# Kernel tuning notes

Hardware: AMD Instinct MI355X
Metric: run time of the kernel (lower is better)

The kernel has to match this reference:

```python
import jax, jax.numpy as jnp
import numpy as np

B, H, S, DH = 2, 16, 2048, 64

def setup_inputs() -> dict:
    key = jax.random.key(0)
    k1, k2, k3 = jax.random.split(key, 3)
    return {
        "query": jax.random.normal(k1, (B, H, S, DH), dtype=jnp.float32),
        "key": jax.random.normal(k2, (B, H, S, DH), dtype=jnp.float32),
        "value": jax.random.normal(k3, (B, H, S, DH), dtype=jnp.float32),
        "key_padding_mask": jnp.zeros((B, S), dtype=bool),
    }

def reference(query, key, value, key_padding_mask):
    # scores: [B, H, Sq, Sk]
    scale = 1.0 / jnp.sqrt(jnp.asarray(query.shape[-1], query.dtype))
    scores = jnp.einsum("bhqd,bhkd->bhqk", query, key) * scale
    # key padding mask broadcasts over heads and query positions
    scores = jnp.where(key_padding_mask[:, None, None, :], -jnp.inf, scores)
    attn = jax.nn.softmax(scores, axis=-1)
    # dropout is identity in eval mode (deterministic reference)
    out = jnp.einsum("bhqk,bhkd->bhqd", attn, value)
    # [B, H, S, Dh] -> [B, S, H*Dh]
    b, h, s, dh = out.shape
    return out.transpose(0, 2, 1, 3).reshape(b, s, h * dh)
```

## Files before the change

### kernel.cpp

```cpp
#include <hip/hip_runtime.h>

typedef __attribute__((ext_vector_type(4))) float f32x4;
typedef __attribute__((ext_vector_type(4))) short s16x4;
typedef __attribute__((ext_vector_type(8))) short s16x8;

constexpr int Bn = 2, Hn = 16, Sn = 2048, DHn = 64;
constexpr int TQ = 64;
constexpr int TK = 64;
constexpr int NT = Sn / TK;
constexpr int TILE_SH = TK * DHn;
constexpr float SHIFT = 16.0f;

__device__ __forceinline__ unsigned pk2(float a, float b) {
  unsigned ua = __builtin_bit_cast(unsigned, a);
  unsigned ub = __builtin_bit_cast(unsigned, b);
  ua += 0x7fffu + ((ua >> 16) & 1u);
  ub += 0x7fffu + ((ub >> 16) & 1u);
  return (ua >> 16) | (ub & 0xffff0000u);
}

__device__ __forceinline__ unsigned cvtpk(float a, float b) {
  unsigned r;
  asm("v_cvt_pk_bf16_f32 %0, %1, %2" : "=v"(r) : "v"(a), "v"(b));
  return r;
}

__device__ __forceinline__ float fexp2(float x) {
#if __has_builtin(__builtin_amdgcn_exp2f)
  return __builtin_amdgcn_exp2f(x);
#else
  return exp2f(x);
#endif
}

__device__ __forceinline__ f32x4 mfma16(s16x4 a, s16x4 b, f32x4 c) {
#if __has_builtin(__builtin_amdgcn_mfma_f32_16x16x16bf16_1k)
  return __builtin_amdgcn_mfma_f32_16x16x16bf16_1k(a, b, c, 0, 0, 0);
#else
  asm("v_mfma_f32_16x16x16_bf16 %0, %1, %2, %0" : "+v"(c) : "v"(a), "v"(b));
  return c;
#endif
}

__global__ __launch_bounds__(256)
void prepack_kernel(const float* __restrict__ Kg, const float* __restrict__ Vg,
                    short* __restrict__ Kp, short* __restrict__ Vp) {
  const int blk = blockIdx.x;
  const int tid = threadIdx.x;
  const float* Kt = Kg + (size_t)blk * TILE_SH;
  const float* Vt = Vg + (size_t)blk * TILE_SH;
  short* Kd = Kp + (size_t)blk * TILE_SH;
  short* Vd = Vp + (size_t)blk * TILE_SH;

  {
    const int r = tid >> 2;
    const int cb = (tid & 3) * 2;
#pragma unroll
    for (int cc = 0; cc < 2; ++cc) {
      int c = cb + cc;
      const float4* p = (const float4*)(Kt + (size_t)r * DHn + c * 8);
      float4 x = p[0], y = p[1];
      union { unsigned u[4]; s16x8 v; } tmp;
      tmp.u[0] = pk2(x.x, x.y); tmp.u[1] = pk2(x.z, x.w);
      tmp.u[2] = pk2(y.x, y.y); tmp.u[3] = pk2(y.z, y.w);
      *(s16x8*)&Kd[r * 64 + (c ^ (r & 7)) * 8] = tmp.v;
    }
  }
  {
    const int d = tid & 63;
    const int kb = (tid >> 6) * 16;
#pragma unroll
    for (int cc = 0; cc < 2; ++cc) {
      int k0 = kb + cc * 8;
      float v0[8];
#pragma unroll
      for (int j = 0; j < 8; ++j) v0[j] = Vt[(size_t)(k0 + j) * DHn + d];
      union { unsigned u[4]; s16x8 v; } tmp;
      tmp.u[0] = pk2(v0[0], v0[1]); tmp.u[1] = pk2(v0[2], v0[3]);
      tmp.u[2] = pk2(v0[4], v0[5]); tmp.u[3] = pk2(v0[6], v0[7]);
      int c = k0 >> 3;
      *(s16x8*)&Vd[d * 64 + (c ^ (d & 7)) * 8] = tmp.v;
    }
  }
}

__global__ __launch_bounds__(256, 4)
void fattn_kernel(const float* __restrict__ Qg, const short* __restrict__ Kp,
                  const short* __restrict__ Vp, const unsigned char* __restrict__ maskg,
                  float* __restrict__ Og) {
  __shared__ __align__(16) float Obuf[TQ * DHn];
  __shared__ float Lb[2][TQ];

  const int tid  = threadIdx.x;
  const int w    = tid >> 6;
  const int lane = tid & 63;
  const int n    = lane & 15;
  const int q4   = lane >> 4;
  const int swz  = n & 7;
  const int wk   = w & 1;
  const int wq   = w >> 1;

  const int blk = blockIdx.x;
  const int bh  = blk & 31;
  const int qt  = blk >> 5;
  const int b   = bh >> 4;
  const int h   = bh & 15;

  const float* Qb = Qg + (size_t)bh * Sn * DHn;
  const short* Kt = Kp + (size_t)bh * NT * TILE_SH;
  const short* Vt = Vp + (size_t)bh * NT * TILE_SH;
  const unsigned char* mq = maskg + (size_t)b * Sn;

  const int q0w = qt * TQ + wq * 32;
  const int t0  = qt & (NT - 1);

  const float c1 = 0.125f * 1.4426950408889634f;
  s16x8 qf[2][2];
#pragma unroll
  for (int qg = 0; qg < 2; ++qg) {
    const float* qrow = Qb + (size_t)(q0w + qg * 16 + n) * DHn;
#pragma unroll
    for (int kc = 0; kc < 2; ++kc) {
      const float4* p = (const float4*)(qrow + kc * 32 + q4 * 8);
      float4 x = p[0], y = p[1];
      union { unsigned u[4]; s16x8 v; } tmp;
      tmp.u[0] = pk2(x.x * c1, x.y * c1);
      tmp.u[1] = pk2(x.z * c1, x.w * c1);
      tmp.u[2] = pk2(y.x * c1, y.y * c1);
      tmp.u[3] = pk2(y.z * c1, y.w * c1);
      qf[qg][kc] = tmp.v;
    }
  }

  const int c0    = q4 ^ swz;
  const int offA  = n * 64 + c0 * 8;
  const int offB  = n * 64 + (c0 ^ 4) * 8;
  const int kbase = wk * 2048;
  const int vsub = (q4 & 1) * 4;
  const int vch0 = (((wk * 4) + (q4 >> 1)) ^ swz) * 8;
  const int vch1 = (((wk * 4) + 2 + (q4 >> 1)) ^ swz) * 8;
  const int mb0  = wk * 32 + q4 * 4;

  f32x4 Oa[2][4];
#pragma unroll
  for (int qg = 0; qg < 2; ++qg)
#pragma unroll
    for (int na = 0; na < 4; ++na) Oa[qg][na] = (f32x4){0.f, 0.f, 0.f, 0.f};
  float lsum[2] = {0.f, 0.f};

  unsigned m0 = *(const unsigned*)&mq[t0 * 64 + mb0];
  unsigned m1 = *(const unsigned*)&mq[t0 * 64 + mb0 + 16];

  for (int i = 0; i < NT; ++i) {
    const int t = (t0 + i) & (NT - 1);
    const short* Ktile = Kt + (size_t)t * TILE_SH;
    const short* Vtile = Vt + (size_t)t * TILE_SH;

    s16x8 kf[2][2];
#pragma unroll
    for (int mc = 0; mc < 2; ++mc) {
      kf[mc][0] = *(const s16x8*)&Ktile[kbase + mc * 1024 + offA];
      kf[mc][1] = *(const s16x8*)&Ktile[kbase + mc * 1024 + offB];
    }
    s16x4 vf[4][2];
#pragma unroll
    for (int na = 0; na < 4; ++na) {
      vf[na][0] = *(const s16x4*)&Vtile[na * 1024 + n * 64 + vch0 + vsub];
      vf[na][1] = *(const s16x4*)&Vtile[na * 1024 + n * 64 + vch1 + vsub];
    }

    const int tn = (t0 + i + 1) & (NT - 1);
    const unsigned mn0 = *(const unsigned*)&mq[tn * 64 + mb0];
    const unsigned mn1 = *(const unsigned*)&mq[tn * 64 + mb0 + 16];

    f32x4 sa[2][2];
#pragma unroll
    for (int r = 0; r < 4; ++r) {
      float b0 = ((m0 >> (8 * r)) & 0xffu) ? -1e30f : -SHIFT;
      float b1 = ((m1 >> (8 * r)) & 0xffu) ? -1e30f : -SHIFT;
      sa[0][0][r] = b0; sa[0][1][r] = b1;
      sa[1][0][r] = b0; sa[1][1][r] = b1;
    }

    __builtin_amdgcn_s_setprio(1);
#pragma unroll
    for (int qg = 0; qg < 2; ++qg)
#pragma unroll
      for (int mc = 0; mc < 2; ++mc)
#pragma unroll
        for (int kc = 0; kc < 2; ++kc)
          sa[qg][mc] = __builtin_amdgcn_mfma_f32_16x16x32_bf16(kf[mc][kc], qf[qg][kc], sa[qg][mc], 0, 0, 0);
    __builtin_amdgcn_s_setprio(0);

    s16x4 pa[2][2];
#pragma unroll
    for (int qg = 0; qg < 2; ++qg) {
#pragma unroll
      for (int mc = 0; mc < 2; ++mc) {
        float p0 = fexp2(sa[qg][mc][0]);
        float p1 = fexp2(sa[qg][mc][1]);
        float p2 = fexp2(sa[qg][mc][2]);
        float p3 = fexp2(sa[qg][mc][3]);
        lsum[qg] += (p0 + p1) + (p2 + p3);
        union { unsigned u[2]; s16x4 v4; } pw;
        pw.u[0] = cvtpk(p0, p1);
        pw.u[1] = cvtpk(p2, p3);
        pa[qg][mc] = pw.v4;
      }
    }

    __builtin_amdgcn_s_setprio(1);
#pragma unroll
    for (int qg = 0; qg < 2; ++qg)
#pragma unroll
      for (int na = 0; na < 4; ++na)
#pragma unroll
        for (int mc = 0; mc < 2; ++mc)
          Oa[qg][na] = mfma16(pa[qg][mc], vf[na][mc], Oa[qg][na]);
    __builtin_amdgcn_s_setprio(0);

    m0 = mn0;
    m1 = mn1;
  }

  lsum[0] += __shfl_xor(lsum[0], 16); lsum[0] += __shfl_xor(lsum[0], 32);
  lsum[1] += __shfl_xor(lsum[1], 16); lsum[1] += __shfl_xor(lsum[1], 32);
  if (lane < 16) {
    Lb[wk][wq * 32 + lane]      = lsum[0];
    Lb[wk][wq * 32 + 16 + lane] = lsum[1];
  }
  if (wk == 1) {
#pragma unroll
    for (int qg = 0; qg < 2; ++qg)
#pragma unroll
      for (int r = 0; r < 4; ++r) {
        const int ql = wq * 32 + qg * 16 + q4 * 4 + r;
#pragma unroll
        for (int na = 0; na < 4; ++na)
          Obuf[ql * 64 + na * 16 + n] = Oa[qg][na][r];
      }
  }
  __syncthreads();
  if (wk == 0) {
#pragma unroll
    for (int qg = 0; qg < 2; ++qg) {
#pragma unroll
      for (int r = 0; r < 4; ++r) {
        const int ql = wq * 32 + qg * 16 + q4 * 4 + r;
        const float inv = 1.0f / (Lb[0][ql] + Lb[1][ql]);
        const int q = qt * TQ + ql;
        float* orow = Og + (size_t)(b * Sn + q) * (Hn * DHn) + h * DHn;
#pragma unroll
        for (int na = 0; na < 4; ++na)
          orow[na * 16 + n] = (Oa[qg][na][r] + Obuf[ql * 64 + na * 16 + n]) * inv;
      }
    }
  }
}

extern "C" void kernel_launch(void* const* d_in, const int* in_sizes, int n_in,
                              void* d_out, int out_size, void* d_ws, size_t ws_size,
                              hipStream_t stream) {
  (void)in_sizes; (void)n_in; (void)ws_size; (void)out_size;
  const float* Q = (const float*)d_in[0];
  const float* K = (const float*)d_in[1];
  const float* V = (const float*)d_in[2];
  const unsigned char* mask = (const unsigned char*)d_in[3];
  float* out = (float*)d_out;

  short* Kp = (short*)d_ws;
  short* Vp = Kp + (size_t)Bn * Hn * Sn * DHn;

  hipLaunchKernelGGL(prepack_kernel, dim3(Bn * Hn * NT), dim3(256), 0, stream, K, V, Kp, Vp);
  hipLaunchKernelGGL(fattn_kernel, dim3(Bn * Hn * (Sn / TQ)), dim3(256), 0, stream,
                     Q, Kp, Vp, mask, out);
}
```

Baseline: 169.6 us.

## Stage K/V tiles through LDS with double-buffered async global-to-LDS loads

Instead of each wave reading packed K/V fragments straight from global memory every iteration, each wave now streams its half of the next-but-one K/V tile into a private LDS double buffer using global_load_lds. Explicit waitcnt fences and sched barriers overlap those loads with the MFMA work. The mask row is also staged in LDS, and V is prepacked in a new 32-wide swizzled layout to match. This aims to hide global load latency, but it adds a lot of LDS (four ~18KB regions) and drops launch bounds occupancy from 4 to 2. The per-wave buffers mean each wave fetches its own copy, and the manual vmcnt accounting is fragile.

```diff
diff --git a/kernel.cpp b/kernel.cpp
--- a/kernel.cpp
+++ b/kernel.cpp
@@ -9,6 +9,7 @@
 constexpr int TK = 64;
 constexpr int NT = Sn / TK;
 constexpr int TILE_SH = TK * DHn;
+constexpr int WREG = 9216;
 constexpr float SHIFT = 16.0f;
 
 __device__ __forceinline__ unsigned pk2(float a, float b) {
@@ -31,6 +32,12 @@
 #else
   return exp2f(x);
 #endif
+}
+
+__device__ __forceinline__ void gl2lds16(const short* g, short* l) {
+  __builtin_amdgcn_global_load_lds(
+      (const __attribute__((address_space(1))) void*)g,
+      (__attribute__((address_space(3))) void*)l, 16, 0, 0);
 }
 
 __device__ __forceinline__ f32x4 mfma16(s16x4 a, s16x4 b, f32x4 c) {
@@ -78,25 +85,24 @@
       union { unsigned u[4]; s16x8 v; } tmp;
       tmp.u[0] = pk2(v0[0], v0[1]); tmp.u[1] = pk2(v0[2], v0[3]);
       tmp.u[2] = pk2(v0[4], v0[5]); tmp.u[3] = pk2(v0[6], v0[7]);
-      int c = k0 >> 3;
-      *(s16x8*)&Vd[d * 64 + (c ^ (d & 7)) * 8] = tmp.v;
-    }
-  }
-}
-
-__global__ __launch_bounds__(256, 4)
+      const int h  = k0 >> 5;
+      const int c2 = (k0 >> 3) & 3;
+      *(s16x8*)&Vd[h * 2048 + d * 32 + ((c2 ^ (d & 3)) * 8)] = tmp.v;
+    }
+  }
+}
+
+__global__ __launch_bounds__(256, 2)
 void fattn_kernel(const float* __restrict__ Qg, const short* __restrict__ Kp,
                   const short* __restrict__ Vp, const unsigned char* __restrict__ maskg,
                   float* __restrict__ Og) {
-  __shared__ __align__(16) float Obuf[TQ * DHn];
-  __shared__ float Lb[2][TQ];
+  __shared__ __align__(16) short Sall[4 * WREG];
 
   const int tid  = threadIdx.x;
   const int w    = tid >> 6;
   const int lane = tid & 63;
   const int n    = lane & 15;
   const int q4   = lane >> 4;
-  const int swz  = n & 7;
   const int wk   = w & 1;
   const int wq   = w >> 1;
 
@@ -113,6 +119,9 @@
 
   const int q0w = qt * TQ + wq * 32;
   const int t0  = qt & (NT - 1);
+
+  short* Wb = &Sall[w * WREG];
+  const unsigned char* Mw = (const unsigned char*)(Wb + 8192);
 
   const float c1 = 0.125f * 1.4426950408889634f;
   s16x8 qf[2][2];
@@ -132,13 +141,15 @@
     }
   }
 
-  const int c0    = q4 ^ swz;
-  const int offA  = n * 64 + c0 * 8;
-  const int offB  = n * 64 + (c0 ^ 4) * 8;
-  const int kbase = wk * 2048;
+  const int swz  = n & 7;
+  const int c0   = q4 ^ swz;
+  const int offA = n * 64 + c0 * 8;
+  const int offB = n * 64 + (c0 ^ 4) * 8;
+  const int vrow = n * 32;
+  const int vq   = q4 >> 1;
   const int vsub = (q4 & 1) * 4;
-  const int vch0 = (((wk * 4) + (q4 >> 1)) ^ swz) * 8;
-  const int vch1 = (((wk * 4) + 2 + (q4 >> 1)) ^ swz) * 8;
+  const int vch0 = ((vq ^ (n & 3)) * 8) + vsub;
+  const int vch1 = (((2 + vq) ^ (n & 3)) * 8) + vsub;
   const int mb0  = wk * 32 + q4 * 4;
 
   f32x4 Oa[2][4];
@@ -148,30 +159,72 @@
     for (int na = 0; na < 4; ++na) Oa[qg][na] = (f32x4){0.f, 0.f, 0.f, 0.f};
   float lsum[2] = {0.f, 0.f};
 
-  unsigned m0 = *(const unsigned*)&mq[t0 * 64 + mb0];
-  unsigned m1 = *(const unsigned*)&mq[t0 * 64 + mb0 + 16];
+  asm volatile("s_waitcnt vmcnt(0)" ::: "memory");
+#pragma unroll
+  for (int k = 0; k < 2; ++k)
+    gl2lds16((const short*)mq + k * 512 + lane * 8, Wb + 8192 + k * 512);
+  {
+    const short* Ktile = Kt + (size_t)t0 * TILE_SH;
+    const short* Vtile = Vt + (size_t)t0 * TILE_SH;
+#pragma unroll
+    for (int k = 0; k < 4; ++k)
+      gl2lds16(Ktile + wk * 2048 + k * 512 + lane * 8, Wb + k * 512);
+#pragma unroll
+    for (int k = 0; k < 4; ++k)
+      gl2lds16(Vtile + wk * 2048 + k * 512 + lane * 8, Wb + 2048 + k * 512);
+  }
+  {
+    const int t1 = (t0 + 1) & (NT - 1);
+    const short* Ktile = Kt + (size_t)t1 * TILE_SH;
+    const short* Vtile = Vt + (size_t)t1 * TILE_SH;
+#pragma unroll
+    for (int k = 0; k < 4; ++k)
+      gl2lds16(Ktile + wk * 2048 + k * 512 + lane * 8, Wb + 4096 + k * 512);
+#pragma unroll
+    for (int k = 0; k < 4; ++k)
+      gl2lds16(Vtile + wk * 2048 + k * 512 + lane * 8, Wb + 4096 + 2048 + k * 512);
+  }
+  asm volatile("s_waitcnt vmcnt(8)" ::: "memory");
+  __builtin_amdgcn_sched_barrier(0);
+
+  unsigned m0 = *(const unsigned*)&Mw[t0 * 64 + mb0];
+  unsigned m1 = *(const unsigned*)&Mw[t0 * 64 + mb0 + 16];
 
   for (int i = 0; i < NT; ++i) {
-    const int t = (t0 + i) & (NT - 1);
-    const short* Ktile = Kt + (size_t)t * TILE_SH;
-    const short* Vtile = Vt + (size_t)t * TILE_SH;
+    const int cur = i & 1;
+    const short* Ks = Wb + cur * 4096;
+    const short* Vs = Ks + 2048;
 
     s16x8 kf[2][2];
 #pragma unroll
     for (int mc = 0; mc < 2; ++mc) {
-      kf[mc][0] = *(const s16x8*)&Ktile[kbase + mc * 1024 + offA];
-      kf[mc][1] = *(const s16x8*)&Ktile[kbase + mc * 1024 + offB];
+      kf[mc][0] = *(const s16x8*)&Ks[mc * 1024 + offA];
+      kf[mc][1] = *(const s16x8*)&Ks[mc * 1024 + offB];
     }
     s16x4 vf[4][2];
 #pragma unroll
     for (int na = 0; na < 4; ++na) {
-      vf[na][0] = *(const s16x4*)&Vtile[na * 1024 + n * 64 + vch0 + vsub];
-      vf[na][1] = *(const s16x4*)&Vtile[na * 1024 + n * 64 + vch1 + vsub];
-    }
-
+      vf[na][0] = *(const s16x4*)&Vs[na * 512 + vrow + vch0];
+      vf[na][1] = *(const s16x4*)&Vs[na * 512 + vrow + vch1];
+    }
     const int tn = (t0 + i + 1) & (NT - 1);
-    const unsigned mn0 = *(const unsigned*)&mq[tn * 64 + mb0];
-    const unsigned mn1 = *(const unsigned*)&mq[tn * 64 + mb0 + 16];
+    const unsigned mn0 = *(const unsigned*)&Mw[tn * 64 + mb0];
+    const unsigned mn1 = *(const unsigned*)&Mw[tn * 64 + mb0 + 16];
+
+    asm volatile("s_waitcnt lgkmcnt(0)" ::: "memory");
+    __builtin_amdgcn_sched_barrier(0);
+
+    {
+      const int ts = (t0 + i + 2) & (NT - 1);
+      const short* Ktile = Kt + (size_t)ts * TILE_SH;
+      const short* Vtile = Vt + (size_t)ts * TILE_SH;
+#pragma unroll
+      for (int k = 0; k < 4; ++k)
+        gl2lds16(Ktile + wk * 2048 + k * 512 + lane * 8, (short*)Ks + k * 512);
+#pragma unroll
+      for (int k = 0; k < 4; ++k)
+        gl2lds16(Vtile + wk * 2048 + k * 512 + lane * 8, (short*)Vs + k * 512);
+    }
 
     f32x4 sa[2][2];
 #pragma unroll
@@ -219,15 +272,22 @@
           Oa[qg][na] = mfma16(pa[qg][mc], vf[na][mc], Oa[qg][na]);
     __builtin_amdgcn_s_setprio(0);
 
+    asm volatile("s_waitcnt vmcnt(8)" ::: "memory");
     m0 = mn0;
     m1 = mn1;
   }
+
+  asm volatile("s_waitcnt vmcnt(0)" ::: "memory");
+  __syncthreads();
+
+  float* Obuf = (float*)Sall;
+  float* Lbf  = (float*)Sall + TQ * DHn;
 
   lsum[0] += __shfl_xor(lsum[0], 16); lsum[0] += __shfl_xor(lsum[0], 32);
   lsum[1] += __shfl_xor(lsum[1], 16); lsum[1] += __shfl_xor(lsum[1], 32);
   if (lane < 16) {
-    Lb[wk][wq * 32 + lane]      = lsum[0];
-    Lb[wk][wq * 32 + 16 + lane] = lsum[1];
+    Lbf[wk * TQ + wq * 32 + lane]      = lsum[0];
+    Lbf[wk * TQ + wq * 32 + 16 + lane] = lsum[1];
   }
   if (wk == 1) {
 #pragma unroll
@@ -247,7 +307,7 @@
 #pragma unroll
       for (int r = 0; r < 4; ++r) {
         const int ql = wq * 32 + qg * 16 + q4 * 4 + r;
-        const float inv = 1.0f / (Lb[0][ql] + Lb[1][ql]);
+        const float inv = 1.0f / (Lbf[ql] + Lbf[TQ + ql]);
         const int q = qt * TQ + ql;
         float* orow = Og + (size_t)(b * Sn + q) * (Hn * DHn) + h * DHn;
 #pragma unroll
```

Result: faster. 153.7 us (-9.4%).

## Stage K/V tiles in LDS via double-buffered async global_load_lds with 512 threads

Applied to the files above, without the earlier changes.

Each attention block now uses 8 waves of 16 query rows each instead of 4 waves of 32 rows. K and V tiles are copied into double-buffered shared memory with async global-to-LDS loads, and the mask row is staged in LDS too. Previously every wave read K/V fragments straight from global memory each iteration. The goal is to share tile loads across waves and overlap the next tile's fetch with compute, at the cost of two barriers per iteration and more LDS per block.

```diff
diff --git a/kernel.cpp b/kernel.cpp
--- a/kernel.cpp
+++ b/kernel.cpp
@@ -31,6 +31,12 @@
 #else
   return exp2f(x);
 #endif
+}
+
+__device__ __forceinline__ void gl2lds16(const short* g, short* l) {
+  __builtin_amdgcn_global_load_lds(
+      (const __attribute__((address_space(1))) void*)g,
+      (__attribute__((address_space(3))) void*)l, 16, 0, 0);
 }
 
 __device__ __forceinline__ f32x4 mfma16(s16x4 a, s16x4 b, f32x4 c) {
@@ -84,12 +90,15 @@
   }
 }
 
-__global__ __launch_bounds__(256, 4)
+__global__ __launch_bounds__(512, 8)
 void fattn_kernel(const float* __restrict__ Qg, const short* __restrict__ Kp,
                   const short* __restrict__ Vp, const unsigned char* __restrict__ maskg,
                   float* __restrict__ Og) {
-  __shared__ __align__(16) float Obuf[TQ * DHn];
-  __shared__ float Lb[2][TQ];
+  __shared__ __align__(16) short Sall[17920];
+  short* Kbuf = Sall;
+  short* Vbuf = Sall + 8192;
+  unsigned char* Mshb = (unsigned char*)(Sall + 16384);
+  float* Lbf = (float*)(Sall + 17408);
 
   const int tid  = threadIdx.x;
   const int w    = tid >> 6;
@@ -111,14 +120,13 @@
   const short* Vt = Vp + (size_t)bh * NT * TILE_SH;
   const unsigned char* mq = maskg + (size_t)b * Sn;
 
-  const int q0w = qt * TQ + wq * 32;
+  const int q0w = qt * TQ + wq * 16;
   const int t0  = qt & (NT - 1);
 
   const float c1 = 0.125f * 1.4426950408889634f;
-  s16x8 qf[2][2];
-#pragma unroll
-  for (int qg = 0; qg < 2; ++qg) {
-    const float* qrow = Qb + (size_t)(q0w + qg * 16 + n) * DHn;
+  s16x8 qf[2];
+  {
+    const float* qrow = Qb + (size_t)(q0w + n) * DHn;
 #pragma unroll
     for (int kc = 0; kc < 2; ++kc) {
       const float4* p = (const float4*)(qrow + kc * 32 + q4 * 8);
@@ -128,7 +136,7 @@
       tmp.u[1] = pk2(x.z * c1, x.w * c1);
       tmp.u[2] = pk2(y.x * c1, y.y * c1);
       tmp.u[3] = pk2(y.z * c1, y.w * c1);
-      qf[qg][kc] = tmp.v;
+      qf[kc] = tmp.v;
     }
   }
 
@@ -136,124 +144,137 @@
   const int offA  = n * 64 + c0 * 8;
   const int offB  = n * 64 + (c0 ^ 4) * 8;
   const int kbase = wk * 2048;
-  const int vsub = (q4 & 1) * 4;
-  const int vch0 = (((wk * 4) + (q4 >> 1)) ^ swz) * 8;
-  const int vch1 = (((wk * 4) + 2 + (q4 >> 1)) ^ swz) * 8;
-  const int mb0  = wk * 32 + q4 * 4;
-
-  f32x4 Oa[2][4];
-#pragma unroll
-  for (int qg = 0; qg < 2; ++qg)
-#pragma unroll
-    for (int na = 0; na < 4; ++na) Oa[qg][na] = (f32x4){0.f, 0.f, 0.f, 0.f};
-  float lsum[2] = {0.f, 0.f};
-
-  unsigned m0 = *(const unsigned*)&mq[t0 * 64 + mb0];
-  unsigned m1 = *(const unsigned*)&mq[t0 * 64 + mb0 + 16];
+  const int vsub  = (q4 & 1) * 4;
+  const int vch0  = (((wk * 4) + (q4 >> 1)) ^ swz) * 8 + vsub;
+  const int vch1  = (((wk * 4) + 2 + (q4 >> 1)) ^ swz) * 8 + vsub;
+  const int mb0   = wk * 32 + q4 * 4;
+
+  f32x4 Oa[4];
+#pragma unroll
+  for (int na = 0; na < 4; ++na) Oa[na] = (f32x4){0.f, 0.f, 0.f, 0.f};
+  float lsum = 0.f;
+
+  asm volatile("s_waitcnt vmcnt(0)" ::: "memory");
+  if (w < 2)
+    gl2lds16((const short*)mq + w * 512 + lane * 8, (short*)Mshb + w * 512);
+  {
+    const short* Ktile = Kt + (size_t)t0 * TILE_SH;
+    const short* Vtile = Vt + (size_t)t0 * TILE_SH;
+    gl2lds16(Ktile + tid * 8, Kbuf + w * 512);
+    gl2lds16(Vtile + tid * 8, Vbuf + w * 512);
+  }
+  {
+    const int t1 = (t0 + 1) & (NT - 1);
+    const short* Ktile = Kt + (size_t)t1 * TILE_SH;
+    const short* Vtile = Vt + (size_t)t1 * TILE_SH;
+    gl2lds16(Ktile + tid * 8, Kbuf + 4096 + w * 512);
+    gl2lds16(Vtile + tid * 8, Vbuf + 4096 + w * 512);
+  }
+  asm volatile("s_waitcnt vmcnt(2)\n\ts_barrier" ::: "memory");
+
+  unsigned m0 = *(const unsigned*)&Mshb[t0 * 64 + mb0];
+  unsigned m1 = *(const unsigned*)&Mshb[t0 * 64 + mb0 + 16];
 
   for (int i = 0; i < NT; ++i) {
-    const int t = (t0 + i) & (NT - 1);
-    const short* Ktile = Kt + (size_t)t * TILE_SH;
-    const short* Vtile = Vt + (size_t)t * TILE_SH;
+    const int cur = i & 1;
+    const short* Ks = Kbuf + cur * 4096;
+    const short* Vs = Vbuf + cur * 4096;
 
     s16x8 kf[2][2];
 #pragma unroll
     for (int mc = 0; mc < 2; ++mc) {
-      kf[mc][0] = *(const s16x8*)&Ktile[kbase + mc * 1024 + offA];
-      kf[mc][1] = *(const s16x8*)&Ktile[kbase + mc * 1024 + offB];
-    }
+      kf[mc][0] = *(const s16x8*)&Ks[kbase + mc * 1024 + offA];
+      kf[mc][1] = *(const s16x8*)&Ks[kbase + mc * 1024 + offB];
+    }
+    const int tn = (t0 + i + 1) & (NT - 1);
+    const unsigned mn0 = *(const unsigned*)&Mshb[tn * 64 + mb0];
+    const unsigned mn1 = *(const unsigned*)&Mshb[tn * 64 + mb0 + 16];
+
+    f32x4 sa[2];
+#pragma unroll
+    for (int r = 0; r < 4; ++r) {
+      sa[0][r] = ((m0 >> (8 * r)) & 0xffu) ? -1e30f : -SHIFT;
+      sa[1][r] = ((m1 >> (8 * r)) & 0xffu) ? -1e30f : -SHIFT;
+    }
+
+    __builtin_amdgcn_s_setprio(1);
+#pragma unroll
+    for (int mc = 0; mc < 2; ++mc)
+#pragma unroll
+      for (int kc = 0; kc < 2; ++kc)
+        sa[mc] = __builtin_amdgcn_mfma_f32_16x16x32_bf16(kf[mc][kc], qf[kc], sa[mc], 0, 0, 0);
+    __builtin_amdgcn_s_setprio(0);
+
+    s16x4 pa[2];
+#pragma unroll
+    for (int mc = 0; mc < 2; ++mc) {
+      float p0 = fexp2(sa[mc][0]);
+      float p1 = fexp2(sa[mc][1]);
+      float p2 = fexp2(sa[mc][2]);
+      float p3 = fexp2(sa[mc][3]);
+      lsum += (p0 + p1) + (p2 + p3);
+      union { unsigned u[2]; s16x4 v4; } pw;
+      pw.u[0] = cvtpk(p0, p1);
+      pw.u[1] = cvtpk(p2, p3);
+      pa[mc] = pw.v4;
+    }
+
     s16x4 vf[4][2];
 #pragma unroll
     for (int na = 0; na < 4; ++na) {
-      vf[na][0] = *(const s16x4*)&Vtile[na * 1024 + n * 64 + vch0 + vsub];
-      vf[na][1] = *(const s16x4*)&Vtile[na * 1024 + n * 64 + vch1 + vsub];
-    }
-
-    const int tn = (t0 + i + 1) & (NT - 1);
-    const unsigned mn0 = *(const unsigned*)&mq[tn * 64 + mb0];
-    const unsigned mn1 = *(const unsigned*)&mq[tn * 64 + mb0 + 16];
-
-    f32x4 sa[2][2];
-#pragma unroll
-    for (int r = 0; r < 4; ++r) {
-      float b0 = ((m0 >> (8 * r)) & 0xffu) ? -1e30f : -SHIFT;
-      float b1 = ((m1 >> (8 * r)) & 0xffu) ? -1e30f : -SHIFT;
-      sa[0][0][r] = b0; sa[0][1][r] = b1;
-      sa[1][0][r] = b0; sa[1][1][r] = b1;
+      vf[na][0] = *(const s16x4*)&Vs[na * 1024 + n * 64 + vch0];
+      vf[na][1] = *(const s16x4*)&Vs[na * 1024 + n * 64 + vch1];
     }
 
     __builtin_amdgcn_s_setprio(1);
 #pragma unroll
-    for (int qg = 0; qg < 2; ++qg)
+    for (int na = 0; na < 4; ++na)
 #pragma unroll
       for (int mc = 0; mc < 2; ++mc)
-#pragma unroll
-        for (int kc = 0; kc < 2; ++kc)
-          sa[qg][mc] = __builtin_amdgcn_mfma_f32_16x16x32_bf16(kf[mc][kc], qf[qg][kc], sa[qg][mc], 0, 0, 0);
+        Oa[na] = mfma16(pa[mc], vf[na][mc], Oa[na]);
     __builtin_amdgcn_s_setprio(0);
 
-    s16x4 pa[2][2];
-#pragma unroll
-    for (int qg = 0; qg < 2; ++qg) {
-#pragma unroll
-      for (int mc = 0; mc < 2; ++mc) {
-        float p0 = fexp2(sa[qg][mc][0]);
-        float p1 = fexp2(sa[qg][mc][1]);
-        float p2 = fexp2(sa[qg][mc][2]);
-        float p3 = fexp2(sa[qg][mc][3]);
-        lsum[qg] += (p0 + p1) + (p2 + p3);
-        union { unsigned u[2]; s16x4 v4; } pw;
-        pw.u[0] = cvtpk(p0, p1);
-        pw.u[1] = cvtpk(p2, p3);
-        pa[qg][mc] = pw.v4;
-      }
-    }
-
-    __builtin_amdgcn_s_setprio(1);
-#pragma unroll
-    for (int qg = 0; qg < 2; ++qg)
-#pragma unroll
-      for (int na = 0; na < 4; ++na)
-#pragma unroll
-        for (int mc = 0; mc < 2; ++mc)
-          Oa[qg][na] = mfma16(pa[qg][mc], vf[na][mc], Oa[qg][na]);
-    __builtin_amdgcn_s_setprio(0);
+    asm volatile("s_waitcnt lgkmcnt(0)\n\ts_barrier" ::: "memory");
+
+    {
+      const int ts = (t0 + i + 2) & (NT - 1);
+      gl2lds16(Kt + (size_t)ts * TILE_SH + tid * 8, (short*)Ks + w * 512);
+      gl2lds16(Vt + (size_t)ts * TILE_SH + tid * 8, (short*)Vs + w * 512);
+    }
+    asm volatile("s_waitcnt vmcnt(2)\n\ts_barrier" ::: "memory");
 
     m0 = mn0;
     m1 = mn1;
   }
 
-  lsum[0] += __shfl_xor(lsum[0], 16); lsum[0] += __shfl_xor(lsum[0], 32);
-  lsum[1] += __shfl_xor(lsum[1], 16); lsum[1] += __shfl_xor(lsum[1], 32);
-  if (lane < 16) {
-    Lb[wk][wq * 32 + lane]      = lsum[0];
-    Lb[wk][wq * 32 + 16 + lane] = lsum[1];
-  }
+  asm volatile("s_waitcnt vmcnt(0)" ::: "memory");
+  __syncthreads();
+
+  lsum += __shfl_xor(lsum, 16);
+  lsum += __shfl_xor(lsum, 32);
+  if (lane < 16) Lbf[wk * 64 + wq * 16 + lane] = lsum;
+
+  float* Obuf = (float*)Sall;
   if (wk == 1) {
 #pragma unroll
-    for (int qg = 0; qg < 2; ++qg)
-#pragma unroll
-      for (int r = 0; r < 4; ++r) {
-        const int ql = wq * 32 + qg * 16 + q4 * 4 + r;
-#pragma unroll
-        for (int na = 0; na < 4; ++na)
-          Obuf[ql * 64 + na * 16 + n] = Oa[qg][na][r];
-      }
+    for (int r = 0; r < 4; ++r) {
+      const int ql = wq * 16 + q4 * 4 + r;
+#pragma unroll
+      for (int na = 0; na < 4; ++na)
+        Obuf[ql * 64 + na * 16 + n] = Oa[na][r];
+    }
   }
   __syncthreads();
   if (wk == 0) {
 #pragma unroll
-    for (int qg = 0; qg < 2; ++qg) {
-#pragma unroll
-      for (int r = 0; r < 4; ++r) {
-        const int ql = wq * 32 + qg * 16 + q4 * 4 + r;
-        const float inv = 1.0f / (Lb[0][ql] + Lb[1][ql]);
-        const int q = qt * TQ + ql;
-        float* orow = Og + (size_t)(b * Sn + q) * (Hn * DHn) + h * DHn;
-#pragma unroll
-        for (int na = 0; na < 4; ++na)
-          orow[na * 16 + n] = (Oa[qg][na][r] + Obuf[ql * 64 + na * 16 + n]) * inv;
-      }
+    for (int r = 0; r < 4; ++r) {
+      const int ql = wq * 16 + q4 * 4 + r;
+      const float inv = 1.0f / (Lbf[ql] + Lbf[64 + ql]);
+      const int q = qt * TQ + ql;
+      float* orow = Og + (size_t)(b * Sn + q) * (Hn * DHn) + h * DHn;
+#pragma unroll
+      for (int na = 0; na < 4; ++na)
+        orow[na * 16 + n] = (Oa[na][r] + Obuf[ql * 64 + na * 16 + n]) * inv;
     }
   }
 }
@@ -272,6 +293,6 @@
   short* Vp = Kp + (size_t)Bn * Hn * Sn * DHn;
 
   hipLaunchKernelGGL(prepack_kernel, dim3(Bn * Hn * NT), dim3(256), 0, stream, K, V, Kp, Vp);
-  hipLaunchKernelGGL(fattn_kernel, dim3(Bn * Hn * (Sn / TQ)), dim3(256), 0, stream,
+  hipLaunchKernelGGL(fattn_kernel, dim3(Bn * Hn * (Sn / TQ)), dim3(512), 0, stream,
                      Q, Kp, Vp, mask, out);
 }
```

Measured after the change: 166.0 us. -2.1%, faster.

## Stage K/V tiles into LDS via async global_load_lds with software-pipelined PV

Applied to the files above, without the earlier changes.

Replaces the direct global loads of packed K/V fragments with double-buffered async global-to-LDS copies, two tiles ahead. The mask is also staged into LDS once. The loop is software-pipelined so the PV MFMA for the previous tile overlaps the exp and QK work of the current tile. The aim is to hide global latency and to let the four waves share tile loads. In exchange it adds a block barrier every iteration and uses more LDS, which may reduce occupancy.

```diff
diff --git a/kernel.cpp b/kernel.cpp
--- a/kernel.cpp
+++ b/kernel.cpp
@@ -31,6 +31,12 @@
 #else
   return exp2f(x);
 #endif
+}
+
+__device__ __forceinline__ void gl2lds16(const short* g, short* l) {
+  __builtin_amdgcn_global_load_lds(
+      (const __attribute__((address_space(1))) void*)g,
+      (__attribute__((address_space(3))) void*)l, 16, 0, 0);
 }
 
 __device__ __forceinline__ f32x4 mfma16(s16x4 a, s16x4 b, f32x4 c) {
@@ -88,8 +94,10 @@
 void fattn_kernel(const float* __restrict__ Qg, const short* __restrict__ Kp,
                   const short* __restrict__ Vp, const unsigned char* __restrict__ maskg,
                   float* __restrict__ Og) {
-  __shared__ __align__(16) float Obuf[TQ * DHn];
-  __shared__ float Lb[2][TQ];
+  __shared__ __align__(16) short KbufS[2 * 4096];
+  __shared__ __align__(16) short VbufS[2 * 4096];
+  __shared__ __align__(16) unsigned char Msh[Sn];
+  __shared__ float Lb[2 * TQ];
 
   const int tid  = threadIdx.x;
   const int w    = tid >> 6;
@@ -136,10 +144,10 @@
   const int offA  = n * 64 + c0 * 8;
   const int offB  = n * 64 + (c0 ^ 4) * 8;
   const int kbase = wk * 2048;
-  const int vsub = (q4 & 1) * 4;
-  const int vch0 = (((wk * 4) + (q4 >> 1)) ^ swz) * 8;
-  const int vch1 = (((wk * 4) + 2 + (q4 >> 1)) ^ swz) * 8;
-  const int mb0  = wk * 32 + q4 * 4;
+  const int vsub  = (q4 & 1) * 4;
+  const int vch0  = (((wk * 4) + (q4 >> 1)) ^ swz) * 8;
+  const int vch1  = (((wk * 4) + 2 + (q4 >> 1)) ^ swz) * 8;
+  const int mb0   = wk * 32 + q4 * 4;
 
   f32x4 Oa[2][4];
 #pragma unroll
@@ -148,32 +156,44 @@
     for (int na = 0; na < 4; ++na) Oa[qg][na] = (f32x4){0.f, 0.f, 0.f, 0.f};
   float lsum[2] = {0.f, 0.f};
 
-  unsigned m0 = *(const unsigned*)&mq[t0 * 64 + mb0];
-  unsigned m1 = *(const unsigned*)&mq[t0 * 64 + mb0 + 16];
-
-  for (int i = 0; i < NT; ++i) {
-    const int t = (t0 + i) & (NT - 1);
-    const short* Ktile = Kt + (size_t)t * TILE_SH;
-    const short* Vtile = Vt + (size_t)t * TILE_SH;
-
+  s16x4 vfA[4][2], vfB[4][2];
+  s16x4 paA[2][2], paB[2][2];
+  f32x4 sa[2][2];
+
+  auto stage_tile = [&](int g, int slot) {
+    const int ts = (t0 + g) & (NT - 1);
+    const short* Ktile = Kt + (size_t)ts * TILE_SH;
+    const short* Vtile = Vt + (size_t)ts * TILE_SH;
+#pragma unroll
+    for (int k = 0; k < 2; ++k) {
+      gl2lds16(Ktile + k * 2048 + tid * 8, &KbufS[slot * 4096 + k * 2048 + w * 512]);
+      gl2lds16(Vtile + k * 2048 + tid * 8, &VbufS[slot * 4096 + k * 2048 + w * 512]);
+    }
+  };
+
+  asm volatile("s_waitcnt vmcnt(0)" ::: "memory");
+  if (w < 2)
+    gl2lds16((const short*)mq + w * 512 + lane * 8, (short*)Msh + w * 512);
+  stage_tile(0, 0);
+  stage_tile(1, 1);
+  asm volatile("s_waitcnt vmcnt(0)\n\ts_barrier" ::: "memory");
+
+  {
+    const short* Ks = &KbufS[0];
+    const short* Vs = &VbufS[0];
     s16x8 kf[2][2];
 #pragma unroll
     for (int mc = 0; mc < 2; ++mc) {
-      kf[mc][0] = *(const s16x8*)&Ktile[kbase + mc * 1024 + offA];
-      kf[mc][1] = *(const s16x8*)&Ktile[kbase + mc * 1024 + offB];
-    }
-    s16x4 vf[4][2];
+      kf[mc][0] = *(const s16x8*)&Ks[kbase + mc * 1024 + offA];
+      kf[mc][1] = *(const s16x8*)&Ks[kbase + mc * 1024 + offB];
+    }
 #pragma unroll
     for (int na = 0; na < 4; ++na) {
-      vf[na][0] = *(const s16x4*)&Vtile[na * 1024 + n * 64 + vch0 + vsub];
-      vf[na][1] = *(const s16x4*)&Vtile[na * 1024 + n * 64 + vch1 + vsub];
-    }
-
-    const int tn = (t0 + i + 1) & (NT - 1);
-    const unsigned mn0 = *(const unsigned*)&mq[tn * 64 + mb0];
-    const unsigned mn1 = *(const unsigned*)&mq[tn * 64 + mb0 + 16];
-
-    f32x4 sa[2][2];
+      vfB[na][0] = *(const s16x4*)&Vs[na * 1024 + n * 64 + vch0 + vsub];
+      vfB[na][1] = *(const s16x4*)&Vs[na * 1024 + n * 64 + vch1 + vsub];
+    }
+    const unsigned m0 = *(const unsigned*)&Msh[t0 * 64 + mb0];
+    const unsigned m1 = *(const unsigned*)&Msh[t0 * 64 + mb0 + 16];
 #pragma unroll
     for (int r = 0; r < 4; ++r) {
       float b0 = ((m0 >> (8 * r)) & 0xffu) ? -1e30f : -SHIFT;
@@ -181,7 +201,6 @@
       sa[0][0][r] = b0; sa[0][1][r] = b1;
       sa[1][0][r] = b0; sa[1][1][r] = b1;
     }
-
     __builtin_amdgcn_s_setprio(1);
 #pragma unroll
     for (int qg = 0; qg < 2; ++qg)
@@ -191,8 +210,10 @@
         for (int kc = 0; kc < 2; ++kc)
           sa[qg][mc] = __builtin_amdgcn_mfma_f32_16x16x32_bf16(kf[mc][kc], qf[qg][kc], sa[qg][mc], 0, 0, 0);
     __builtin_amdgcn_s_setprio(0);
-
-    s16x4 pa[2][2];
+  }
+
+  auto body = [&](int i, s16x4 (&vfP)[4][2], s16x4 (&paP)[2][2], s16x4 (&paC)[2][2]) {
+    __builtin_amdgcn_s_setprio(1);
 #pragma unroll
     for (int qg = 0; qg < 2; ++qg) {
 #pragma unroll
@@ -205,30 +226,87 @@
         union { unsigned u[2]; s16x4 v4; } pw;
         pw.u[0] = cvtpk(p0, p1);
         pw.u[1] = cvtpk(p2, p3);
-        pa[qg][mc] = pw.v4;
-      }
-    }
-
-    __builtin_amdgcn_s_setprio(1);
-#pragma unroll
-    for (int qg = 0; qg < 2; ++qg)
-#pragma unroll
-      for (int na = 0; na < 4; ++na)
+        paC[qg][mc] = pw.v4;
+      }
+    }
+    if (i != 0) {
+#pragma unroll
+      for (int qg = 0; qg < 2; ++qg)
+#pragma unroll
+        for (int na = 0; na < 4; ++na)
+#pragma unroll
+          for (int mc = 0; mc < 2; ++mc)
+            Oa[qg][na] = mfma16(paP[qg][mc], vfP[na][mc], Oa[qg][na]);
+    }
+    __builtin_amdgcn_s_setprio(0);
+
+    asm volatile("s_waitcnt vmcnt(0) lgkmcnt(0)\n\ts_barrier" ::: "memory");
+
+    stage_tile(i + 2, i & 1);
+
+    {
+      const short* Ks = &KbufS[((i + 1) & 1) * 4096];
+      const short* Vs = &VbufS[((i + 1) & 1) * 4096];
+      s16x8 kf[2][2];
+#pragma unroll
+      for (int mc = 0; mc < 2; ++mc) {
+        kf[mc][0] = *(const s16x8*)&Ks[kbase + mc * 1024 + offA];
+        kf[mc][1] = *(const s16x8*)&Ks[kbase + mc * 1024 + offB];
+      }
+#pragma unroll
+      for (int na = 0; na < 4; ++na) {
+        vfP[na][0] = *(const s16x4*)&Vs[na * 1024 + n * 64 + vch0 + vsub];
+        vfP[na][1] = *(const s16x4*)&Vs[na * 1024 + n * 64 + vch1 + vsub];
+      }
+      const int tn = (t0 + i + 1) & (NT - 1);
+      const unsigned m0 = *(const unsigned*)&Msh[tn * 64 + mb0];
+      const unsigned m1 = *(const unsigned*)&Msh[tn * 64 + mb0 + 16];
+
+#pragma unroll
+      for (int r = 0; r < 4; ++r) {
+        float b0 = ((m0 >> (8 * r)) & 0xffu) ? -1e30f : -SHIFT;
+        float b1 = ((m1 >> (8 * r)) & 0xffu) ? -1e30f : -SHIFT;
+        sa[0][0][r] = b0; sa[0][1][r] = b1;
+        sa[1][0][r] = b0; sa[1][1][r] = b1;
+      }
+      __builtin_amdgcn_s_setprio(1);
+#pragma unroll
+      for (int qg = 0; qg < 2; ++qg)
 #pragma unroll
         for (int mc = 0; mc < 2; ++mc)
-          Oa[qg][na] = mfma16(pa[qg][mc], vf[na][mc], Oa[qg][na]);
-    __builtin_amdgcn_s_setprio(0);
-
-    m0 = mn0;
-    m1 = mn1;
-  }
+#pragma unroll
+          for (int kc = 0; kc < 2; ++kc)
+            sa[qg][mc] = __builtin_amdgcn_mfma_f32_16x16x32_bf16(kf[mc][kc], qf[qg][kc], sa[qg][mc], 0, 0, 0);
+      __builtin_amdgcn_s_setprio(0);
+    }
+  };
+
+#pragma unroll 1
+  for (int i = 0; i < NT; i += 2) {
+    body(i,     vfA, paB, paA);
+    body(i + 1, vfB, paA, paB);
+  }
+
+  __builtin_amdgcn_s_setprio(1);
+#pragma unroll
+  for (int qg = 0; qg < 2; ++qg)
+#pragma unroll
+    for (int na = 0; na < 4; ++na)
+#pragma unroll
+      for (int mc = 0; mc < 2; ++mc)
+        Oa[qg][na] = mfma16(paB[qg][mc], vfA[na][mc], Oa[qg][na]);
+  __builtin_amdgcn_s_setprio(0);
+
+  asm volatile("s_waitcnt vmcnt(0)" ::: "memory");
+  __syncthreads();
 
   lsum[0] += __shfl_xor(lsum[0], 16); lsum[0] += __shfl_xor(lsum[0], 32);
   lsum[1] += __shfl_xor(lsum[1], 16); lsum[1] += __shfl_xor(lsum[1], 32);
   if (lane < 16) {
-    Lb[wk][wq * 32 + lane]      = lsum[0];
-    Lb[wk][wq * 32 + 16 + lane] = lsum[1];
-  }
+    Lb[wk * TQ + wq * 32 + lane]      = lsum[0];
+    Lb[wk * TQ + wq * 32 + 16 + lane] = lsum[1];
+  }
+  float* Obuf = (float*)&KbufS[0];
   if (wk == 1) {
 #pragma unroll
     for (int qg = 0; qg < 2; ++qg)
@@ -247,7 +325,7 @@
 #pragma unroll
       for (int r = 0; r < 4; ++r) {
         const int ql = wq * 32 + qg * 16 + q4 * 4 + r;
-        const float inv = 1.0f / (Lb[0][ql] + Lb[1][ql]);
+        const float inv = 1.0f / (Lb[ql] + Lb[TQ + ql]);
         const int q = qt * TQ + ql;
         float* orow = Og + (size_t)(b * Sn + q) * (Hn * DHn) + h * DHn;
 #pragma unroll
```

Measured after the change: 272.7 us. 1.61x slower.
